# Optimization experiments

Measured on AMD Instinct MI355X. Metric: run time of the kernel, lower is better.

The kernel has to match this reference:

```python
import jax, jax.numpy as jnp
import numpy as np

B, N, D, N_HOPS = 32, 1024, 128, 3
EPS = 1e-6


def setup_inputs() -> dict:
    key = jax.random.key(0)
    k1, k2, k3, k4 = jax.random.split(key, 4)
    # binary base adjacency (non-trainable buffer in the torch module)
    adj = (jax.random.uniform(k1, (N, N)) < 0.05).astype(jnp.float32)
    adj_weight = jax.random.uniform(k2, (B, N, N), dtype=jnp.float32)
    x = jax.random.normal(k3, (B, N, D), dtype=jnp.float32)
    W = jax.random.normal(k4, (D, D), dtype=jnp.float32) * 0.05
    b = jnp.zeros((D,), jnp.float32)
    a2 = jnp.ones((D,), jnp.float32)   # LayerNorm scale
    b2 = jnp.zeros((D,), jnp.float32)  # LayerNorm shift
    return {"x": x, "adj_weight": adj_weight, "adj": adj, "W": W, "b": b, "a2": a2, "b2": b2}


def _conv(x, adj_weight, adj):
    # adj_power squares the matrix each hop: hop h uses A^(2^h).
    # mask_h = (A^(2^h) == 1.0); weighted hop = (W^(2^h)) * mask_h.
    # propagate(edge_index from dense_to_sparse) == sum_j Wmask[b,j,i] * x[b,j]  (A^T x)
    A = adj            # [N, N]
    Wp = adj_weight    # [B, N, N]
    agg = jnp.zeros_like(x)
    for h in range(N_HOPS):
        mask = (A == 1.0).astype(x.dtype)          # [N, N]
        Wh = Wp * mask                              # [B, N, N]
        agg = agg + jnp.einsum('bji,bjd->bid', Wh, x)
        if h < N_HOPS - 1:
            A = A @ A
            Wp = jnp.matmul(Wp, Wp)
    return agg


def reference(x, adj_weight, adj, W, b, a2, b2):
    agg = _conv(x, adj_weight, adj)
    h = jnp.einsum('bnd,od->bno', agg, W) + b + x   # Linear + residual
    mean = jnp.mean(h, axis=-1, keepdims=True)
    std = jnp.std(h, axis=-1, keepdims=True, ddof=1)  # torch.std is unbiased
    y = a2 * (h - mean) / (std + EPS) + b2
    return y  # dropout p=0 (eval) -> identity
```

## Files before the change

### kernel.cpp

```cpp
#include <hip/hip_runtime.h>

#define NN 1024
#define BB 32
#define DD 128
#define EPSF 1e-6f
#define CAP 16384
#define NNNN ((size_t)NN * NN)

typedef __bf16 bf16x8 __attribute__((ext_vector_type(8)));
typedef float  f32x4  __attribute__((ext_vector_type(4)));
typedef unsigned short u16x8 __attribute__((ext_vector_type(8)));

typedef __attribute__((address_space(3))) unsigned int lds_u32;
typedef __attribute__((address_space(1))) const unsigned int glb_u32;

__device__ __forceinline__ lds_u32* lds_cast(const void* p) {
  return (lds_u32*)(unsigned int)(unsigned long long)p;
}
__device__ __forceinline__ glb_u32* glb_cast(const void* p) {
  return (glb_u32*)(unsigned long long)p;
}

__device__ __forceinline__ float bf2f(unsigned short u) {
  union { unsigned int i; float f; } v; v.i = ((unsigned int)u) << 16; return v.f;
}
__device__ __forceinline__ unsigned short f2bf(float f) {
  union { float f; unsigned int i; } v; v.f = f;
  unsigned int r = v.i + 0x7fffu + ((v.i >> 16) & 1u);
  return (unsigned short)(r >> 16);
}


__global__ __launch_bounds__(256) void convert_wp(const float* __restrict__ src,
    unsigned short* __restrict__ Wp, unsigned short* __restrict__ WpT) {
  __shared__ float tile[64][65];
  const int b = blockIdx.z;
  const int c0 = blockIdx.x * 64, r0 = blockIdx.y * 64;
  const int t = threadIdx.x;
  const int rr = t >> 3, cb = (t & 7) * 8;
  const size_t base = (size_t)b * NNNN;
#pragma unroll
  for (int p = 0; p < 2; ++p) {
    const int r = rr + p * 32;
    const float* srow = src + base + (size_t)(r0 + r) * NN + c0 + cb;
    f32x4 v0 = *(const f32x4*)srow;
    f32x4 v1 = *(const f32x4*)(srow + 4);
    u16x8 w;
#pragma unroll
    for (int j = 0; j < 4; ++j) { w[j] = f2bf(v0[j]); w[4 + j] = f2bf(v1[j]); }
    *(u16x8*)(Wp + base + (size_t)(r0 + r) * NN + c0 + cb) = w;
#pragma unroll
    for (int j = 0; j < 4; ++j) { tile[r][cb + j] = v0[j]; tile[r][cb + 4 + j] = v1[j]; }
  }
  __syncthreads();
#pragma unroll
  for (int p = 0; p < 2; ++p) {
    const int r = rr + p * 32;
    u16x8 w;
#pragma unroll
    for (int j = 0; j < 8; ++j) w[j] = f2bf(tile[cb + j][r]);
    *(u16x8*)(WpT + base + (size_t)(c0 + r) * NN + r0 + cb) = w;
  }
}

__global__ __launch_bounds__(256) void convert_x(const float* __restrict__ x,
    unsigned short* __restrict__ xT) {
  __shared__ float tile[32][33];
  const int b = blockIdx.z;
  const int d0 = blockIdx.x * 32, n0 = blockIdx.y * 32;
  const int tx = threadIdx.x, ty = threadIdx.y;
#pragma unroll
  for (int s = 0; s < 4; ++s) {
    int rr = ty + s * 8;
    tile[rr][tx] = x[(size_t)b * NN * DD + (size_t)(n0 + rr) * DD + d0 + tx];
  }
  __syncthreads();
#pragma unroll
  for (int s = 0; s < 4; ++s) {
    int rr = ty + s * 8;
    xT[(size_t)b * DD * NN + (size_t)(d0 + rr) * NN + n0 + tx] = f2bf(tile[tx][rr]);
  }
}

__global__ __launch_bounds__(256) void mask0cvt(const float* __restrict__ adj,
    unsigned char* __restrict__ mcode, unsigned short* __restrict__ adjbf,
    unsigned short* __restrict__ adjTbf) {
  __shared__ float tile[32][33];
  const int i0 = blockIdx.x * 32, j0 = blockIdx.y * 32;
  const int tx = threadIdx.x, ty = threadIdx.y;
#pragma unroll
  for (int s = 0; s < 4; ++s) {
    int rr = ty + s * 8;
    float v = adj[(size_t)(j0 + rr) * NN + i0 + tx];
    adjbf[(size_t)(j0 + rr) * NN + i0 + tx] = f2bf(v);
    tile[rr][tx] = v;
  }
  __syncthreads();
#pragma unroll
  for (int s = 0; s < 4; ++s) {
    int rr = ty + s * 8;
    float v = tile[tx][rr];
    adjTbf[(size_t)(i0 + rr) * NN + j0 + tx] = f2bf(v);
    mcode[(size_t)(i0 + rr) * NN + j0 + tx] = (v == 1.0f) ? 1 : 0;
  }
}

__global__ __launch_bounds__(256) void scan_a2(const float* __restrict__ P,
    unsigned short* __restrict__ A2, unsigned short* __restrict__ A2T,
    unsigned char* __restrict__ mcode) {
  __shared__ float tile[32][33];
  const int m0 = blockIdx.x * 32, n0 = blockIdx.y * 32;
  const int tx = threadIdx.x, ty = threadIdx.y;
#pragma unroll
  for (int s = 0; s < 4; ++s) {
    int rr = ty + s * 8;
    size_t idx = (size_t)(m0 + rr) * NN + n0 + tx;
    float v = P[idx] + P[NNNN + idx] + P[2 * NNNN + idx] + P[3 * NNNN + idx];
    A2[idx] = f2bf(v);
    tile[rr][tx] = v;
  }
  __syncthreads();
#pragma unroll
  for (int s = 0; s < 4; ++s) {
    int rr = ty + s * 8;
    float v = tile[tx][rr];
    A2T[(size_t)(n0 + rr) * NN + m0 + tx] = f2bf(v);
    if (v == 1.0f) mcode[(size_t)(n0 + rr) * NN + m0 + tx] |= 2;
  }
}

__global__ __launch_bounds__(256) void scan_a4(const float* __restrict__ P,
    unsigned int* __restrict__ entries, int* __restrict__ nnz) {
  size_t e = (size_t)blockIdx.x * 256 + threadIdx.x;
  float v = P[e] + P[NNNN + e] + P[2 * NNNN + e] + P[3 * NNNN + e];
  if (v == 1.0f) {
    int idx = atomicAdd(nnz, 1);
    if (idx < CAP) entries[idx] = ((unsigned)(e >> 10) << 16) | (unsigned)(e & 1023);
  }
}

#define BM 128
#define BN 128
#define BK 32

struct EpiWcomb {
  const unsigned char* mc;
  unsigned short* out;
  __device__ __forceinline__ void operator()(int b, int ks, int i, int j, float v) const {
    size_t idx = (size_t)i * NN + j;
    out[(size_t)b * NNNN + idx] = (mc[idx] & 2) ? f2bf(v) : (unsigned short)0;
  }
};

struct EpiSqPart {
  float* buf;
  __device__ __forceinline__ void operator()(int b, int ks, int i, int j, float v) const {
    buf[(size_t)ks * NNNN + (size_t)i * NN + j] = v;
  }
};

struct EpiAggPart {
  float* p0;
  float* p1;
  __device__ __forceinline__ void operator()(int b, int ks, int i, int d, float v) const {
    (ks ? p1 : p0)[(size_t)b * NN * DD + (size_t)i * DD + d] = v;
  }
};

#define LGKM_BARRIER() do { \
  asm volatile("s_waitcnt lgkmcnt(0)" ::: "memory"); \
  __builtin_amdgcn_s_barrier(); \
  asm volatile("" ::: "memory"); } while (0)

template <int MW, typename Epi>
__global__ __launch_bounds__(256, MW) void gemm_lds(
    const unsigned short* __restrict__ Ap, size_t sA,
    const unsigned short* __restrict__ Bp, size_t sB,
    int swz, int ksN, int nit, Epi epi) {
  __shared__ __align__(16) unsigned short As[2 * BM * BK];
  __shared__ __align__(16) unsigned short Bs[2 * BN * BK];
  int bx = blockIdx.x, by = blockIdx.y, z = blockIdx.z;
  if (swz == 1) {
    int lin = bx + (by << 3);
    int r = lin & 7, s = lin >> 3;
    bx = ((r & 3) << 1) | (s & 1);
    by = ((r >> 2) << 2) | (s >> 1);
  } else if (swz == 2) {
    int lin = bx + (by << 3) + (z << 6);
    int xcd = lin & 7, q = lin >> 3;
    z = xcd + ((q >> 6) << 3);
    int tile = q & 63;
    bx = tile & 7; by = tile >> 3;
  }
  const int b = z / ksN, ks = z - b * ksN;
  const int kbase = ks * nit * BK;
  const int tm = bx * BM, tn = by * BN;
  const unsigned short* Ab = Ap + (size_t)b * sA;
  const unsigned short* Bb = Bp + (size_t)b * sB;
  const int tid = threadIdx.x;
  const int w = tid >> 6, l = tid & 63;
  const int fr = l & 15, quad = l >> 4;
  const int moff = (w & 1) * 64, noff = (w >> 1) * 64;

  const int sr = l >> 2, ss = l & 3;
  const int r0 = w * 16 + sr;
  const int r1 = 64 + w * 16 + sr;
  const int kc0 = ss ^ ((r0 >> 1) & 3);
  const int kc1 = ss ^ ((r1 >> 1) & 3);
  const unsigned short* gA0 = Ab + (size_t)(tm + r0) * NN + kbase + kc0 * 8;
  const unsigned short* gA1 = Ab + (size_t)(tm + r1) * NN + kbase + kc1 * 8;
  const unsigned short* gB0 = Bb + (size_t)(tn + r0) * NN + kbase + kc0 * 8;
  const unsigned short* gB1 = Bb + (size_t)(tn + r1) * NN + kbase + kc1 * 8;
  lds_u32* const lA0_0 = lds_cast(As + (w * 16) * BK);
  lds_u32* const lA1_0 = lds_cast(As + (64 + w * 16) * BK);
  lds_u32* const lB0_0 = lds_cast(Bs + (w * 16) * BK);
  lds_u32* const lB1_0 = lds_cast(Bs + (64 + w * 16) * BK);
  lds_u32* const lA0_1 = lds_cast(As + BM * BK + (w * 16) * BK);
  lds_u32* const lA1_1 = lds_cast(As + BM * BK + (64 + w * 16) * BK);
  lds_u32* const lB0_1 = lds_cast(Bs + BN * BK + (w * 16) * BK);
  lds_u32* const lB1_1 = lds_cast(Bs + BN * BK + (64 + w * 16) * BK);
  const unsigned short* const As0 = As;            const unsigned short* const As1 = As + BM * BK;
  const unsigned short* const Bs0 = Bs;            const unsigned short* const Bs1 = Bs + BN * BK;

  f32x4 acc[4][4];
#pragma unroll
  for (int mi = 0; mi < 4; ++mi)
#pragma unroll
    for (int ni = 0; ni < 4; ++ni) acc[mi][ni] = (f32x4){0.f, 0.f, 0.f, 0.f};

  auto stage = [&](lds_u32* a0, lds_u32* a1, lds_u32* b0, lds_u32* b1, int kt) {
    const size_t kk = (size_t)kt * BK;
    __builtin_amdgcn_global_load_lds(glb_cast(gA0 + kk), a0, 16, 0, 0);
    __builtin_amdgcn_global_load_lds(glb_cast(gA1 + kk), a1, 16, 0, 0);
    __builtin_amdgcn_global_load_lds(glb_cast(gB0 + kk), b0, 16, 0, 0);
    __builtin_amdgcn_global_load_lds(glb_cast(gB1 + kk), b1, 16, 0, 0);
  };
  auto compute = [&](const unsigned short* Ad, const unsigned short* Bd) {
    bf16x8 af[4], bfr[4];
#pragma unroll
    for (int mi = 0; mi < 4; ++mi) {
      int r = moff + mi * 16 + fr;
      int kc = quad ^ ((r >> 1) & 3);
      af[mi] = *(const bf16x8*)(Ad + r * BK + kc * 8);
    }
#pragma unroll
    for (int ni = 0; ni < 4; ++ni) {
      int r = noff + ni * 16 + fr;
      int kc = quad ^ ((r >> 1) & 3);
      bfr[ni] = *(const bf16x8*)(Bd + r * BK + kc * 8);
    }
#pragma unroll
    for (int mi = 0; mi < 4; ++mi)
#pragma unroll
      for (int ni = 0; ni < 4; ++ni)
        acc[mi][ni] = __builtin_amdgcn_mfma_f32_16x16x32_bf16(af[mi], bfr[ni], acc[mi][ni], 0, 0, 0);
  };

  stage(lA0_0, lA1_0, lB0_0, lB1_0, 0);
  __syncthreads();
#pragma unroll 1
  for (int kt = 0; kt < nit; kt += 2) {
    if (kt + 1 < nit) stage(lA0_1, lA1_1, lB0_1, lB1_1, kt + 1);
    __builtin_amdgcn_sched_barrier(0);
    compute(As0, Bs0);
    __syncthreads();
    if (kt + 1 < nit) {
      if (kt + 2 < nit) stage(lA0_0, lA1_0, lB0_0, lB1_0, kt + 2);
      __builtin_amdgcn_sched_barrier(0);
      compute(As1, Bs1);
      __syncthreads();
    }
  }

#pragma unroll
  for (int mi = 0; mi < 4; ++mi)
#pragma unroll
    for (int ni = 0; ni < 4; ++ni)
#pragma unroll
      for (int t = 0; t < 4; ++t)
        epi(b, ks, tm + moff + mi * 16 + quad * 4 + t, tn + noff + ni * 16 + fr, acc[mi][ni][t]);
}

template <int MW, bool COMB, typename Epi>
__global__ __launch_bounds__(256, MW) void gemm_pipe(
    const unsigned short* __restrict__ Ap, size_t sA,
    const unsigned short* __restrict__ WtP, const unsigned char* __restrict__ McP,
    const unsigned short* __restrict__ Bp, size_t sB,
    int swz, int ksN, int nit, Epi epi) {
  __shared__ __align__(16) unsigned short As[2 * BM * BK];
  __shared__ __align__(16) unsigned short Bs[2 * BN * BK];
  int bx = blockIdx.x, by = blockIdx.y, z = blockIdx.z;
  if (swz == 1) {
    int lin = bx + (by << 3);
    int r = lin & 7, s = lin >> 3;
    bx = ((r & 3) << 1) | (s & 1);
    by = ((r >> 2) << 2) | (s >> 1);
  } else if (swz == 2) {
    int lin = bx + (z << 3);
    int xcd = lin & 7, q = lin >> 3;
    z = (xcd << 3) + (q >> 3);
    bx = q & 7;
  }
  const int b = z / ksN, ks = z - b * ksN;
  const int kbase = ks * nit * BK;
  const int tm = bx * BM, tn = by * BN;
  const unsigned short* Ab = Ap + (size_t)b * sA;
  const unsigned short* Bb = Bp + (size_t)b * sB;
  const unsigned short* Wb = COMB ? (WtP + (size_t)b * sA) : nullptr;
  const int tid = threadIdx.x;
  const int w = tid >> 6, l = tid & 63;
  const int lr = l >> 2, lc = l & 3;
  const int fr = l & 15, quad = l >> 4;
  const int moff = (w & 1) * 64, noff = (w >> 1) * 64;
  const int r0 = w * 16 + lr, r1 = (w + 4) * 16 + lr;
  const int kc0 = lc ^ ((r0 >> 1) & 3), kc1 = lc ^ ((r1 >> 1) & 3);
  const size_t ao0 = (size_t)(tm + r0) * NN + kbase + kc0 * 8;
  const size_t ao1 = (size_t)(tm + r1) * NN + kbase + kc1 * 8;
  const size_t bo0 = (size_t)(tn + r0) * NN + kbase + kc0 * 8;
  const size_t bo1 = (size_t)(tn + r1) * NN + kbase + kc1 * 8;
  const int ls0 = r0 * BK + lc * 8, ls1 = r1 * BK + lc * 8;

  unsigned short* const As0 = As;           unsigned short* const As1 = As + BM * BK;
  unsigned short* const Bs0 = Bs;           unsigned short* const Bs1 = Bs + BN * BK;

  f32x4 acc[4][4];
#pragma unroll
  for (int mi = 0; mi < 4; ++mi)
#pragma unroll
    for (int ni = 0; ni < 4; ++ni) acc[mi][ni] = (f32x4){0.f, 0.f, 0.f, 0.f};

  struct RegSet {
    u16x8 a0, a1, b0, b1;
    u16x8 w0, w1;
    unsigned long long m0, m1;
  };
  RegSet R0, R1;

  auto load = [&](RegSet& R, int kt) {
    size_t kk = (size_t)kt * BK;
    R.a0 = *(const u16x8*)(Ab + ao0 + kk);
    R.a1 = *(const u16x8*)(Ab + ao1 + kk);
    R.b0 = *(const u16x8*)(Bb + bo0 + kk);
    R.b1 = *(const u16x8*)(Bb + bo1 + kk);
    if constexpr (COMB) {
      R.w0 = *(const u16x8*)(Wb + ao0 + kk);
      R.w1 = *(const u16x8*)(Wb + ao1 + kk);
      R.m0 = *(const unsigned long long*)(McP + ao0 + kk);
      R.m1 = *(const unsigned long long*)(McP + ao1 + kk);
    }
  };
  auto wr = [&](const RegSet& R, unsigned short* Ad, unsigned short* Bd) {
    if constexpr (COMB) {
      u16x8 f0, f1;
#pragma unroll
      for (int j = 0; j < 8; ++j) {
        float s0 = bf2f(R.a0[j]);
        if ((R.m0 >> (8 * j)) & 1ull) s0 += bf2f(R.w0[j]);
        f0[j] = f2bf(s0);
        float s1 = bf2f(R.a1[j]);
        if ((R.m1 >> (8 * j)) & 1ull) s1 += bf2f(R.w1[j]);
        f1[j] = f2bf(s1);
      }
      *(u16x8*)(Ad + ls0) = f0;
      *(u16x8*)(Ad + ls1) = f1;
    } else {
      *(u16x8*)(Ad + ls0) = R.a0;
      *(u16x8*)(Ad + ls1) = R.a1;
    }
    *(u16x8*)(Bd + ls0) = R.b0;
    *(u16x8*)(Bd + ls1) = R.b1;
  };
  auto compute = [&](const unsigned short* Ad, const unsigned short* Bd) {
    bf16x8 af[4], bfr[4];
#pragma unroll
    for (int mi = 0; mi < 4; ++mi) {
      int r = moff + mi * 16 + fr;
      int kc = quad ^ ((r >> 1) & 3);
      af[mi] = *(const bf16x8*)(Ad + r * BK + kc * 8);
    }
#pragma unroll
    for (int ni = 0; ni < 4; ++ni) {
      int r = noff + ni * 16 + fr;
      int kc = quad ^ ((r >> 1) & 3);
      bfr[ni] = *(const bf16x8*)(Bd + r * BK + kc * 8);
    }
#pragma unroll
    for (int mi = 0; mi < 4; ++mi)
#pragma unroll
      for (int ni = 0; ni < 4; ++ni)
        acc[mi][ni] = __builtin_amdgcn_mfma_f32_16x16x32_bf16(af[mi], bfr[ni], acc[mi][ni], 0, 0, 0);
  };

  load(R0, 0);
  load(R1, 1);
  wr(R0, As0, Bs0);
  load(R0, 2);
  LGKM_BARRIER();
#pragma unroll 1
  for (int kt = 0; kt < nit - 2; kt += 2) {
    compute(As0, Bs0);
    wr(R1, As1, Bs1);
    if (kt + 3 < nit) load(R1, kt + 3);
    LGKM_BARRIER();
    compute(As1, Bs1);
    wr(R0, As0, Bs0);
    if (kt + 4 < nit) load(R0, kt + 4);
    LGKM_BARRIER();
  }
  compute(As0, Bs0);
  wr(R1, As1, Bs1);
  LGKM_BARRIER();
  compute(As1, Bs1);

#pragma unroll
  for (int mi = 0; mi < 4; ++mi)
#pragma unroll
    for (int ni = 0; ni < 4; ++ni)
#pragma unroll
      for (int t = 0; t < 4; ++t)
        epi(b, ks, tm + moff + mi * 16 + quad * 4 + t, tn + noff + ni * 16 + fr, acc[mi][ni][t]);
}

__global__ __launch_bounds__(256) void hop2_fix(const unsigned short* __restrict__ Wp,
    const unsigned short* __restrict__ WpT, const int* __restrict__ nnz,
    const unsigned int* __restrict__ entries, unsigned short* __restrict__ WcombT) {
  int n = *nnz;
  if (n > CAP) n = CAP;
  if (n == 0) return;
  __shared__ float rbuf[256];
  const int b = blockIdx.x;
  const size_t bnn = (size_t)b * NNNN;
  for (int e = blockIdx.y; e < n; e += gridDim.y) {
    unsigned int ent = entries[e];
    int j = ent >> 16, i = ent & 0xFFFF;
    float s = 0.f;
    for (int k = threadIdx.x; k < NN; k += 256) {
      float u = 0.f, v = 0.f;
      const unsigned short* wj  = Wp  + bnn + (size_t)j * NN;
      const unsigned short* wtk = WpT + bnn + (size_t)k * NN;
      const unsigned short* wk  = Wp  + bnn + (size_t)k * NN;
      const unsigned short* wti = WpT + bnn + (size_t)i * NN;
      for (int t = 0; t < NN; ++t) {
        u += bf2f(wj[t]) * bf2f(wtk[t]);
        v += bf2f(wk[t]) * bf2f(wti[t]);
      }
      s += u * v;
    }
    rbuf[threadIdx.x] = s;
    __syncthreads();
    for (int off = 128; off > 0; off >>= 1) {
      if (threadIdx.x < off) rbuf[threadIdx.x] += rbuf[threadIdx.x + off];
      __syncthreads();
    }
    if (threadIdx.x == 0) {
      size_t idx = bnn + (size_t)i * NN + j;
      WcombT[idx] = f2bf(bf2f(WcombT[idx]) + rbuf[0]);
    }
    __syncthreads();
  }
}

#define FROWS 16
__global__ __launch_bounds__(256) void fused_out(const float* __restrict__ a0p,
    const float* __restrict__ a1p, const float* __restrict__ x,
    const float* __restrict__ W, const float* __restrict__ bias,
    const float* __restrict__ g2, const float* __restrict__ bsh,
    float* __restrict__ out) {
  __shared__ unsigned short Wl[128 * 136];
  __shared__ float ar[256];
  __shared__ float wred[8];
  const int tid = threadIdx.x;
  for (int e = tid; e < 16384; e += 256) Wl[(e >> 7) * 136 + (e & 127)] = f2bf(W[e]);
  const int half = tid >> 7, o = tid & 127;
  const int w = tid >> 6, lane = tid & 63;
  const float bo = bias[o], go = g2[o], b2o = bsh[o];
  const size_t row0 = (size_t)blockIdx.x * FROWS;
  size_t rb = row0 * DD;
  float av = a0p[rb + tid] + a1p[rb + tid];
  float xv = x[rb + tid];
  __syncthreads();
  for (int rr = 0; rr < FROWS; rr += 2) {
    ar[tid] = av;
    const float xcur = xv;
    const size_t rbc = (row0 + rr) * DD;
    __syncthreads();
    if (rr + 2 < FROWS) {
      size_t rb2 = (row0 + rr + 2) * DD;
      av = a0p[rb2 + tid] + a1p[rb2 + tid];
      xv = x[rb2 + tid];
    }
    float hv = bo + xcur;
    const unsigned short* wrow = &Wl[o * 136];
    const float* arow = &ar[half * 128];
#pragma unroll
    for (int d8 = 0; d8 < 16; ++d8) {
      bf16x8 wv = *(const bf16x8*)(wrow + d8 * 8);
#pragma unroll
      for (int t = 0; t < 8; ++t) hv += (float)wv[t] * arow[d8 * 8 + t];
    }
    float s = hv, q = hv * hv;
#pragma unroll
    for (int off = 32; off > 0; off >>= 1) {
      s += __shfl_xor(s, off);
      q += __shfl_xor(q, off);
    }
    if (lane == 0) { wred[w] = s; wred[4 + w] = q; }
    __syncthreads();
    float st = wred[half * 2] + wred[half * 2 + 1];
    float qt = wred[4 + half * 2] + wred[4 + half * 2 + 1];
    float mean = st * (1.0f / 128.0f);
    float var = (qt - 128.0f * mean * mean) * (1.0f / 127.0f);
    var = fmaxf(var, 0.0f);
    float stdv = sqrtf(var);
    out[rbc + tid] = go * (hv - mean) / (stdv + EPSF) + b2o;
  }
}

extern "C" void kernel_launch(void* const* d_in, const int* in_sizes, int n_in,
                              void* d_out, int out_size, void* d_ws, size_t ws_size,
                              hipStream_t stream) {
  (void)in_sizes; (void)n_in; (void)out_size; (void)ws_size;
  const float* x    = (const float*)d_in[0];
  const float* adjw = (const float*)d_in[1];
  const float* adj  = (const float*)d_in[2];
  const float* W    = (const float*)d_in[3];
  const float* bias = (const float*)d_in[4];
  const float* a2   = (const float*)d_in[5];
  const float* b2   = (const float*)d_in[6];
  float* out = (float*)d_out;

  char* ws = (char*)d_ws;
  const size_t MB = 1048576;
  unsigned short* Wp_bf   = (unsigned short*)(ws);
  unsigned short* WpT_bf  = (unsigned short*)(ws + 64 * MB);
  unsigned short* WcombT  = (unsigned short*)(ws + 128 * MB);
  unsigned short* xT_bf   = (unsigned short*)(ws + 192 * MB);
  unsigned short* adj_bf  = (unsigned short*)(ws + 200 * MB);
  unsigned short* adjT_bf = (unsigned short*)(ws + 202 * MB);
  unsigned short* A2_bf   = (unsigned short*)(ws + 204 * MB);
  unsigned short* A2T_bf  = (unsigned short*)(ws + 206 * MB);
  float* sqpart           = (float*)(ws + 208 * MB);
  float* agg1             = (float*)(ws + 200 * MB);
  unsigned char* mcode    = (unsigned char*)(ws + 224 * MB);
  unsigned int* entries   = (unsigned int*)(ws + 225 * MB);
  int* nnz2               = (int*)(ws + 226 * MB);
  float* agg0 = out;

  hipMemsetAsync(nnz2, 0, 4, stream);

  dim3 blk32(32, 8, 1);
  convert_wp<<<dim3(16, 16, 32), 256, 0, stream>>>(adjw, Wp_bf, WpT_bf);
  convert_x<<<dim3(4, 32, 32), blk32, 0, stream>>>(x, xT_bf);
  mask0cvt<<<dim3(32, 32, 1), blk32, 0, stream>>>(adj, mcode, adj_bf, adjT_bf);

  gemm_lds<4><<<dim3(8, 8, 4), 256, 0, stream>>>(
      adj_bf, (size_t)0, adjT_bf, (size_t)0, 0, 4, 8, EpiSqPart{sqpart});
  scan_a2<<<dim3(32, 32, 1), blk32, 0, stream>>>(sqpart, A2_bf, A2T_bf, mcode);
  gemm_lds<4><<<dim3(8, 8, 4), 256, 0, stream>>>(
      A2_bf, (size_t)0, A2T_bf, (size_t)0, 0, 4, 8, EpiSqPart{sqpart});
  scan_a4<<<dim3(4096, 1, 1), 256, 0, stream>>>(sqpart, entries, nnz2);

  gemm_lds<4><<<dim3(8, 8, 32), 256, 0, stream>>>(
      WpT_bf, NNNN, Wp_bf, NNNN, 2, 1, NN / BK, EpiWcomb{mcode, WcombT});

  hop2_fix<<<dim3(32, 8, 1), 256, 0, stream>>>(Wp_bf, WpT_bf, nnz2, entries, WcombT);

  gemm_pipe<2, true><<<dim3(8, 1, 64), 256, 0, stream>>>(
      WcombT, NNNN, WpT_bf, mcode, xT_bf, (size_t)DD * NN, 2, 2, 16,
      EpiAggPart{agg0, agg1});

  fused_out<<<dim3(2048, 1, 1), 256, 0, stream>>>(agg0, agg1, x, W, bias, a2, b2, out);
}
```

Before: 464.3 us.

## Replace 128x128 LDS GEMM with 256x128 tile loading B directly to registers

```diff
diff --git a/kernel.cpp b/kernel.cpp
--- a/kernel.cpp
+++ b/kernel.cpp
@@ -139,9 +139,6 @@
   }
 }
 
-#define BM 128
-#define BN 128
-#define BK 32
 
 struct EpiWcomb {
   const unsigned char* mc;
@@ -172,114 +169,121 @@
   __builtin_amdgcn_s_barrier(); \
   asm volatile("" ::: "memory"); } while (0)
 
+#define GBM 256
+#define GBN 128
+#define GBK 32
+
 template <int MW, typename Epi>
-__global__ __launch_bounds__(256, MW) void gemm_lds(
+__global__ __launch_bounds__(256, MW) void gemm_big(
     const unsigned short* __restrict__ Ap, size_t sA,
     const unsigned short* __restrict__ Bp, size_t sB,
     int swz, int ksN, int nit, Epi epi) {
-  __shared__ __align__(16) unsigned short As[2 * BM * BK];
-  __shared__ __align__(16) unsigned short Bs[2 * BN * BK];
+  __shared__ __align__(16) unsigned short As[2 * GBM * GBK];
   int bx = blockIdx.x, by = blockIdx.y, z = blockIdx.z;
-  if (swz == 1) {
-    int lin = bx + (by << 3);
-    int r = lin & 7, s = lin >> 3;
-    bx = ((r & 3) << 1) | (s & 1);
-    by = ((r >> 2) << 2) | (s >> 1);
-  } else if (swz == 2) {
-    int lin = bx + (by << 3) + (z << 6);
-    int xcd = lin & 7, q = lin >> 3;
-    z = xcd + ((q >> 6) << 3);
-    int tile = q & 63;
-    bx = tile & 7; by = tile >> 3;
+  if (swz == 2) {
+    int lin = bx + (by << 2) + (z << 5);
+    int xcd = lin & 7, rest = lin >> 3;
+    z = (xcd << 2) + (rest >> 5);
+    int tile = rest & 31;
+    bx = tile & 3; by = tile >> 2;
   }
   const int b = z / ksN, ks = z - b * ksN;
-  const int kbase = ks * nit * BK;
-  const int tm = bx * BM, tn = by * BN;
+  const int kbase = ks * nit * GBK;
+  const int tm = bx * GBM, tn = by * GBN;
   const unsigned short* Ab = Ap + (size_t)b * sA;
   const unsigned short* Bb = Bp + (size_t)b * sB;
   const int tid = threadIdx.x;
   const int w = tid >> 6, l = tid & 63;
   const int fr = l & 15, quad = l >> 4;
-  const int moff = (w & 1) * 64, noff = (w >> 1) * 64;
-
-  const int sr = l >> 2, ss = l & 3;
-  const int r0 = w * 16 + sr;
-  const int r1 = 64 + w * 16 + sr;
-  const int kc0 = ss ^ ((r0 >> 1) & 3);
-  const int kc1 = ss ^ ((r1 >> 1) & 3);
-  const unsigned short* gA0 = Ab + (size_t)(tm + r0) * NN + kbase + kc0 * 8;
-  const unsigned short* gA1 = Ab + (size_t)(tm + r1) * NN + kbase + kc1 * 8;
-  const unsigned short* gB0 = Bb + (size_t)(tn + r0) * NN + kbase + kc0 * 8;
-  const unsigned short* gB1 = Bb + (size_t)(tn + r1) * NN + kbase + kc1 * 8;
-  lds_u32* const lA0_0 = lds_cast(As + (w * 16) * BK);
-  lds_u32* const lA1_0 = lds_cast(As + (64 + w * 16) * BK);
-  lds_u32* const lB0_0 = lds_cast(Bs + (w * 16) * BK);
-  lds_u32* const lB1_0 = lds_cast(Bs + (64 + w * 16) * BK);
-  lds_u32* const lA0_1 = lds_cast(As + BM * BK + (w * 16) * BK);
-  lds_u32* const lA1_1 = lds_cast(As + BM * BK + (64 + w * 16) * BK);
-  lds_u32* const lB0_1 = lds_cast(Bs + BN * BK + (w * 16) * BK);
-  lds_u32* const lB1_1 = lds_cast(Bs + BN * BK + (64 + w * 16) * BK);
-  const unsigned short* const As0 = As;            const unsigned short* const As1 = As + BM * BK;
-  const unsigned short* const Bs0 = Bs;            const unsigned short* const Bs1 = Bs + BN * BK;
-
-  f32x4 acc[4][4];
-#pragma unroll
-  for (int mi = 0; mi < 4; ++mi)
+  const int wm = w >> 1, wn = w & 1;
+  const int moff = wm * 128, noff = wn * 64;
+
+  const int srow = l >> 2, gpos = l & 3;
+  const unsigned short* gA[4];
+#pragma unroll
+  for (int i = 0; i < 4; ++i) {
+    int r = i * 64 + w * 16 + srow;
+    int g = gpos ^ ((r >> 1) & 3);
+    gA[i] = Ab + (size_t)(tm + r) * NN + kbase + g * 8;
+  }
+  unsigned short* const As0 = As;
+  unsigned short* const As1 = As + GBM * GBK;
+
+  const size_t bo0 = (size_t)(tn + noff + 0 * 16 + fr) * NN + kbase + quad * 8;
+  const size_t bo1 = (size_t)(tn + noff + 1 * 16 + fr) * NN + kbase + quad * 8;
+  const size_t bo2 = (size_t)(tn + noff + 2 * 16 + fr) * NN + kbase + quad * 8;
+  const size_t bo3 = (size_t)(tn + noff + 3 * 16 + fr) * NN + kbase + quad * 8;
+
+  f32x4 acc[8][4];
+#pragma unroll
+  for (int mi = 0; mi < 8; ++mi)
 #pragma unroll
     for (int ni = 0; ni < 4; ++ni) acc[mi][ni] = (f32x4){0.f, 0.f, 0.f, 0.f};
 
-  auto stage = [&](lds_u32* a0, lds_u32* a1, lds_u32* b0, lds_u32* b1, int kt) {
-    const size_t kk = (size_t)kt * BK;
-    __builtin_amdgcn_global_load_lds(glb_cast(gA0 + kk), a0, 16, 0, 0);
-    __builtin_amdgcn_global_load_lds(glb_cast(gA1 + kk), a1, 16, 0, 0);
-    __builtin_amdgcn_global_load_lds(glb_cast(gB0 + kk), b0, 16, 0, 0);
-    __builtin_amdgcn_global_load_lds(glb_cast(gB1 + kk), b1, 16, 0, 0);
-  };
-  auto compute = [&](const unsigned short* Ad, const unsigned short* Bd) {
-    bf16x8 af[4], bfr[4];
-#pragma unroll
-    for (int mi = 0; mi < 4; ++mi) {
+  struct BReg { bf16x8 v0, v1, v2, v3; };
+  BReg B0, B1;
+
+  auto stageA = [&](unsigned short* Asl, int kt) {
+    const size_t kk = (size_t)kt * GBK;
+#pragma unroll
+    for (int i = 0; i < 4; ++i) {
+      lds_u32* dst = lds_cast(Asl + (i * 64 + w * 16) * GBK);
+      __builtin_amdgcn_global_load_lds(glb_cast(gA[i] + kk), dst, 16, 0, 0);
+    }
+  };
+  auto loadB = [&](BReg& R, int kt) {
+    const size_t kk = (size_t)kt * GBK;
+    R.v0 = *(const bf16x8*)(Bb + bo0 + kk);
+    R.v1 = *(const bf16x8*)(Bb + bo1 + kk);
+    R.v2 = *(const bf16x8*)(Bb + bo2 + kk);
+    R.v3 = *(const bf16x8*)(Bb + bo3 + kk);
+  };
+  auto compute = [&](const unsigned short* Ad, const BReg& R) {
+    bf16x8 af[8];
+#pragma unroll
+    for (int mi = 0; mi < 8; ++mi) {
       int r = moff + mi * 16 + fr;
       int kc = quad ^ ((r >> 1) & 3);
-      af[mi] = *(const bf16x8*)(Ad + r * BK + kc * 8);
-    }
-#pragma unroll
-    for (int ni = 0; ni < 4; ++ni) {
-      int r = noff + ni * 16 + fr;
-      int kc = quad ^ ((r >> 1) & 3);
-      bfr[ni] = *(const bf16x8*)(Bd + r * BK + kc * 8);
-    }
-#pragma unroll
-    for (int mi = 0; mi < 4; ++mi)
-#pragma unroll
-      for (int ni = 0; ni < 4; ++ni)
-        acc[mi][ni] = __builtin_amdgcn_mfma_f32_16x16x32_bf16(af[mi], bfr[ni], acc[mi][ni], 0, 0, 0);
-  };
-
-  stage(lA0_0, lA1_0, lB0_0, lB1_0, 0);
+      af[mi] = *(const bf16x8*)(Ad + r * GBK + kc * 8);
+    }
+#pragma unroll
+    for (int mi = 0; mi < 8; ++mi) {
+      acc[mi][0] = __builtin_amdgcn_mfma_f32_16x16x32_bf16(af[mi], R.v0, acc[mi][0], 0, 0, 0);
+      acc[mi][1] = __builtin_amdgcn_mfma_f32_16x16x32_bf16(af[mi], R.v1, acc[mi][1], 0, 0, 0);
+      acc[mi][2] = __builtin_amdgcn_mfma_f32_16x16x32_bf16(af[mi], R.v2, acc[mi][2], 0, 0, 0);
+      acc[mi][3] = __builtin_amdgcn_mfma_f32_16x16x32_bf16(af[mi], R.v3, acc[mi][3], 0, 0, 0);
+    }
+  };
+
+  stageA(As0, 0);
+  loadB(B0, 0);
   __syncthreads();
 #pragma unroll 1
   for (int kt = 0; kt < nit; kt += 2) {
-    if (kt + 1 < nit) stage(lA0_1, lA1_1, lB0_1, lB1_1, kt + 1);
+    if (kt + 1 < nit) { stageA(As1, kt + 1); loadB(B1, kt + 1); }
     __builtin_amdgcn_sched_barrier(0);
-    compute(As0, Bs0);
+    compute(As0, B0);
     __syncthreads();
     if (kt + 1 < nit) {
-      if (kt + 2 < nit) stage(lA0_0, lA1_0, lB0_0, lB1_0, kt + 2);
+      if (kt + 2 < nit) { stageA(As0, kt + 2); loadB(B0, kt + 2); }
       __builtin_amdgcn_sched_barrier(0);
-      compute(As1, Bs1);
+      compute(As1, B1);
       __syncthreads();
     }
   }
 
 #pragma unroll
-  for (int mi = 0; mi < 4; ++mi)
+  for (int mi = 0; mi < 8; ++mi)
 #pragma unroll
     for (int ni = 0; ni < 4; ++ni)
 #pragma unroll
       for (int t = 0; t < 4; ++t)
         epi(b, ks, tm + moff + mi * 16 + quad * 4 + t, tn + noff + ni * 16 + fr, acc[mi][ni][t]);
 }
+
+#define BM 128
+#define BN 128
+#define BK 32
 
 template <int MW, bool COMB, typename Epi>
 __global__ __launch_bounds__(256, MW) void gemm_pipe(
@@ -553,15 +557,15 @@
   convert_x<<<dim3(4, 32, 32), blk32, 0, stream>>>(x, xT_bf);
   mask0cvt<<<dim3(32, 32, 1), blk32, 0, stream>>>(adj, mcode, adj_bf, adjT_bf);
 
-  gemm_lds<4><<<dim3(8, 8, 4), 256, 0, stream>>>(
+  gemm_big<2><<<dim3(4, 8, 4), 256, 0, stream>>>(
       adj_bf, (size_t)0, adjT_bf, (size_t)0, 0, 4, 8, EpiSqPart{sqpart});
   scan_a2<<<dim3(32, 32, 1), blk32, 0, stream>>>(sqpart, A2_bf, A2T_bf, mcode);
-  gemm_lds<4><<<dim3(8, 8, 4), 256, 0, stream>>>(
+  gemm_big<2><<<dim3(4, 8, 4), 256, 0, stream>>>(
       A2_bf, (size_t)0, A2T_bf, (size_t)0, 0, 4, 8, EpiSqPart{sqpart});
   scan_a4<<<dim3(4096, 1, 1), 256, 0, stream>>>(sqpart, entries, nnz2);
 
-  gemm_lds<4><<<dim3(8, 8, 32), 256, 0, stream>>>(
-      WpT_bf, NNNN, Wp_bf, NNNN, 2, 1, NN / BK, EpiWcomb{mcode, WcombT});
+  gemm_big<2><<<dim3(4, 8, 32), 256, 0, stream>>>(
+      WpT_bf, NNNN, Wp_bf, NNNN, 2, 1, NN / GBK, EpiWcomb{mcode, WcombT});
 
   hop2_fix<<<dim3(32, 8, 1), 256, 0, stream>>>(Wp_bf, WpT_bf, nnz2, entries, WcombT);
 
```

After: 522.2 us. 1.12x slower.

## Triple-buffer LDS in gemm_lds with vmcnt waits and one barrier per step

Applied to the files above, without the earlier changes.

```diff
diff --git a/kernel.cpp b/kernel.cpp
--- a/kernel.cpp
+++ b/kernel.cpp
@@ -177,8 +177,8 @@
     const unsigned short* __restrict__ Ap, size_t sA,
     const unsigned short* __restrict__ Bp, size_t sB,
     int swz, int ksN, int nit, Epi epi) {
-  __shared__ __align__(16) unsigned short As[2 * BM * BK];
-  __shared__ __align__(16) unsigned short Bs[2 * BN * BK];
+  __shared__ __align__(16) unsigned short As[3 * BM * BK];
+  __shared__ __align__(16) unsigned short Bs[3 * BN * BK];
   int bx = blockIdx.x, by = blockIdx.y, z = blockIdx.z;
   if (swz == 1) {
     int lin = bx + (by << 3);
@@ -211,16 +211,6 @@
   const unsigned short* gA1 = Ab + (size_t)(tm + r1) * NN + kbase + kc1 * 8;
   const unsigned short* gB0 = Bb + (size_t)(tn + r0) * NN + kbase + kc0 * 8;
   const unsigned short* gB1 = Bb + (size_t)(tn + r1) * NN + kbase + kc1 * 8;
-  lds_u32* const lA0_0 = lds_cast(As + (w * 16) * BK);
-  lds_u32* const lA1_0 = lds_cast(As + (64 + w * 16) * BK);
-  lds_u32* const lB0_0 = lds_cast(Bs + (w * 16) * BK);
-  lds_u32* const lB1_0 = lds_cast(Bs + (64 + w * 16) * BK);
-  lds_u32* const lA0_1 = lds_cast(As + BM * BK + (w * 16) * BK);
-  lds_u32* const lA1_1 = lds_cast(As + BM * BK + (64 + w * 16) * BK);
-  lds_u32* const lB0_1 = lds_cast(Bs + BN * BK + (w * 16) * BK);
-  lds_u32* const lB1_1 = lds_cast(Bs + BN * BK + (64 + w * 16) * BK);
-  const unsigned short* const As0 = As;            const unsigned short* const As1 = As + BM * BK;
-  const unsigned short* const Bs0 = Bs;            const unsigned short* const Bs1 = Bs + BN * BK;
 
   f32x4 acc[4][4];
 #pragma unroll
@@ -228,12 +218,16 @@
 #pragma unroll
     for (int ni = 0; ni < 4; ++ni) acc[mi][ni] = (f32x4){0.f, 0.f, 0.f, 0.f};
 
-  auto stage = [&](lds_u32* a0, lds_u32* a1, lds_u32* b0, lds_u32* b1, int kt) {
+  auto stage = [&](int off, int kt) {
     const size_t kk = (size_t)kt * BK;
-    __builtin_amdgcn_global_load_lds(glb_cast(gA0 + kk), a0, 16, 0, 0);
-    __builtin_amdgcn_global_load_lds(glb_cast(gA1 + kk), a1, 16, 0, 0);
-    __builtin_amdgcn_global_load_lds(glb_cast(gB0 + kk), b0, 16, 0, 0);
-    __builtin_amdgcn_global_load_lds(glb_cast(gB1 + kk), b1, 16, 0, 0);
+    __builtin_amdgcn_global_load_lds(glb_cast(gA0 + kk),
+        lds_cast(As + off + (w * 16) * BK), 16, 0, 0);
+    __builtin_amdgcn_global_load_lds(glb_cast(gA1 + kk),
+        lds_cast(As + off + (64 + w * 16) * BK), 16, 0, 0);
+    __builtin_amdgcn_global_load_lds(glb_cast(gB0 + kk),
+        lds_cast(Bs + off + (w * 16) * BK), 16, 0, 0);
+    __builtin_amdgcn_global_load_lds(glb_cast(gB1 + kk),
+        lds_cast(Bs + off + (64 + w * 16) * BK), 16, 0, 0);
   };
   auto compute = [&](const unsigned short* Ad, const unsigned short* Bd) {
     bf16x8 af[4], bfr[4];
@@ -256,20 +250,21 @@
         acc[mi][ni] = __builtin_amdgcn_mfma_f32_16x16x32_bf16(af[mi], bfr[ni], acc[mi][ni], 0, 0, 0);
   };
 
-  stage(lA0_0, lA1_0, lB0_0, lB1_0, 0);
-  __syncthreads();
+  stage(0, 0);
+  stage(BM * BK, 1);
+  int o0 = 0, o1 = BM * BK, o2 = 2 * BM * BK;
 #pragma unroll 1
-  for (int kt = 0; kt < nit; kt += 2) {
-    if (kt + 1 < nit) stage(lA0_1, lA1_1, lB0_1, lB1_1, kt + 1);
+  for (int kt = 0; kt < nit; ++kt) {
+    if (kt + 1 < nit) {
+      asm volatile("s_waitcnt vmcnt(4)" ::: "memory");
+    } else {
+      asm volatile("s_waitcnt vmcnt(0)" ::: "memory");
+    }
     __builtin_amdgcn_sched_barrier(0);
-    compute(As0, Bs0);
-    __syncthreads();
-    if (kt + 1 < nit) {
-      if (kt + 2 < nit) stage(lA0_0, lA1_0, lB0_0, lB1_0, kt + 2);
-      __builtin_amdgcn_sched_barrier(0);
-      compute(As1, Bs1);
-      __syncthreads();
-    }
+    __builtin_amdgcn_s_barrier();
+    if (kt + 2 < nit) stage(o2, kt + 2);
+    compute(As + o0, Bs + o0);
+    int t = o0; o0 = o1; o1 = o2; o2 = t;
   }
 
 #pragma unroll
@@ -553,14 +548,14 @@
   convert_x<<<dim3(4, 32, 32), blk32, 0, stream>>>(x, xT_bf);
   mask0cvt<<<dim3(32, 32, 1), blk32, 0, stream>>>(adj, mcode, adj_bf, adjT_bf);
 
-  gemm_lds<4><<<dim3(8, 8, 4), 256, 0, stream>>>(
+  gemm_lds<3><<<dim3(8, 8, 4), 256, 0, stream>>>(
       adj_bf, (size_t)0, adjT_bf, (size_t)0, 0, 4, 8, EpiSqPart{sqpart});
   scan_a2<<<dim3(32, 32, 1), blk32, 0, stream>>>(sqpart, A2_bf, A2T_bf, mcode);
-  gemm_lds<4><<<dim3(8, 8, 4), 256, 0, stream>>>(
+  gemm_lds<3><<<dim3(8, 8, 4), 256, 0, stream>>>(
       A2_bf, (size_t)0, A2T_bf, (size_t)0, 0, 4, 8, EpiSqPart{sqpart});
   scan_a4<<<dim3(4096, 1, 1), 256, 0, stream>>>(sqpart, entries, nnz2);
 
-  gemm_lds<4><<<dim3(8, 8, 32), 256, 0, stream>>>(
+  gemm_lds<3><<<dim3(8, 8, 32), 256, 0, stream>>>(
       WpT_bf, NNNN, Wp_bf, NNNN, 2, 1, NN / BK, EpiWcomb{mcode, WcombT});
 
   hop2_fix<<<dim3(32, 8, 1), 256, 0, stream>>>(Wp_bf, WpT_bf, nnz2, entries, WcombT);
```

Result: slower. 477.6 us (+2.9%).
